# Kernel optimization log

Measured on AMD Instinct MI355X. Metric: run time of the kernel, lower is better.

Reference implementation:

```python
import jax, jax.numpy as jnp
import numpy as np

NEIGHBOR_N = 3


def setup_inputs() -> dict:
    key = jax.random.key(0)
    ks = jax.random.split(key, 4)
    B, D = 8192, 512
    H = D // 2
    sess_emb = jax.random.normal(ks[0], (B, D), dtype=jnp.float32)
    pool_emb = jax.random.normal(ks[1], (1024, D), dtype=jnp.float32)
    # torch Linear default init ~ U(-1/sqrt(fan_in), 1/sqrt(fan_in)); scaled normals ok as baseline
    W1 = jax.random.normal(ks[2], (D, H), dtype=jnp.float32) / np.sqrt(D)
    b1 = jnp.zeros((H,), dtype=jnp.float32)
    W2 = jax.random.normal(ks[3], (H, D), dtype=jnp.float32) / np.sqrt(H)
    b2 = jnp.zeros((D,), dtype=jnp.float32)
    return {"sess_emb": sess_emb, "pool_emb": pool_emb, "W1": W1, "b1": b1, "W2": W2, "b2": b2}


def reference(sess_emb, pool_emb, W1, b1, W2, b2):
    # scoring MLP (dropout = identity in eval mode)
    h = jax.nn.relu(sess_emb @ W1 + b1)          # (B, D/2)
    sess_proj = h @ W2 + b2                       # (B, D)
    # self-similarity and top-k neighbors
    sim_matrix = sess_proj @ sess_proj.T          # (B, B)
    cos_topk, topk_indice = jax.lax.top_k(sim_matrix, NEIGHBOR_N)  # (B, K)
    sess_topk = sess_emb[topk_indice]             # (B, K, D) gather
    cos_topk = jax.nn.softmax(cos_topk, axis=-1)  # (B, K)
    neighbor_sess = jnp.einsum('bk,bkd->bd', cos_topk, sess_topk)  # (B, D)
    return (sess_topk, neighbor_sess, cos_topk)
```

## Files before the change

### kernel.cpp

```cpp
#include <hip/hip_runtime.h>
#include <hip/hip_bf16.h>
#include <math.h>

#define NB 8192
#define DD 512
#define HH 256
#define TB 128
#define BK 32
#define BK2 64
#define KT2 (DD / BK2)
#define NSLOT 64
#define ROWKEYS (NSLOT * 3)
#define NCAND 8
#define NTRI 2080

typedef unsigned short ushortT;
typedef __attribute__((ext_vector_type(8))) short bf16x8;
typedef __attribute__((ext_vector_type(4))) float f32x4;

#define AS1(p) ((const __attribute__((address_space(1))) void*)(p))
#define AS3(p) ((__attribute__((address_space(3))) void*)(p))

__device__ __forceinline__ ushortT bf16rne(float f) {
    unsigned u = __float_as_uint(f);
    unsigned r = u + 0x7FFFu + ((u >> 16) & 1u);
    return (ushortT)(r >> 16);
}
__device__ __forceinline__ float bf16tof(ushortT h) {
    return __uint_as_float(((unsigned)h) << 16);
}

__global__ __launch_bounds__(256)
void prep_kernel(const float* __restrict__ sess, const float* __restrict__ W1,
                 const float* __restrict__ W2,
                 ushortT* __restrict__ sess_hi, ushortT* __restrict__ sess_lo,
                 ushortT* __restrict__ w1t_hi, ushortT* __restrict__ w1t_lo,
                 ushortT* __restrict__ w2t_hi, ushortT* __restrict__ w2t_lo) {
    const int b = blockIdx.x, t = threadIdx.x;
    if (b < 2048) {
        size_t i = (size_t)b * 2048 + t * 8;
        float4 f0 = *(const float4*)&sess[i];
        float4 f1 = *(const float4*)&sess[i + 4];
        float f[8] = {f0.x, f0.y, f0.z, f0.w, f1.x, f1.y, f1.z, f1.w};
        unsigned hp[4], lp[4];
#pragma unroll
        for (int j = 0; j < 4; ++j) {
            ushortT h0 = bf16rne(f[2 * j]), h1 = bf16rne(f[2 * j + 1]);
            ushortT l0 = bf16rne(f[2 * j] - bf16tof(h0));
            ushortT l1 = bf16rne(f[2 * j + 1] - bf16tof(h1));
            hp[j] = (unsigned)h0 | ((unsigned)h1 << 16);
            lp[j] = (unsigned)l0 | ((unsigned)l1 << 16);
        }
        *(uint4*)&sess_hi[i] = *(uint4*)hp;
        *(uint4*)&sess_lo[i] = *(uint4*)lp;
    } else if (b < 2112) {
        int o = (b - 2048) * 2048 + t * 8;
        int k = o >> 8, c = o & 255;
        float4 f0 = *(const float4*)&W1[(size_t)k * 256 + c];
        float4 f1 = *(const float4*)&W1[(size_t)k * 256 + c + 4];
        float f[8] = {f0.x, f0.y, f0.z, f0.w, f1.x, f1.y, f1.z, f1.w};
#pragma unroll
        for (int j = 0; j < 8; ++j) {
            ushortT h = bf16rne(f[j]);
            w1t_hi[(size_t)(c + j) * 512 + k] = h;
            w1t_lo[(size_t)(c + j) * 512 + k] = bf16rne(f[j] - bf16tof(h));
        }
    } else {
        int o = (b - 2112) * 2048 + t * 8;
        int k = o >> 9, c = o & 511;
        float4 f0 = *(const float4*)&W2[(size_t)k * 512 + c];
        float4 f1 = *(const float4*)&W2[(size_t)k * 512 + c + 4];
        float f[8] = {f0.x, f0.y, f0.z, f0.w, f1.x, f1.y, f1.z, f1.w};
#pragma unroll
        for (int j = 0; j < 8; ++j) {
            ushortT h = bf16rne(f[j]);
            w2t_hi[(size_t)(c + j) * 256 + k] = h;
            w2t_lo[(size_t)(c + j) * 256 + k] = bf16rne(f[j] - bf16tof(h));
        }
    }
}

template <int KDIM, int NOUT, int EPI, int TM>
__global__ __launch_bounds__(256)
void mlp_gemm(const ushortT* __restrict__ Ahi, const ushortT* __restrict__ Alo,
              const ushortT* __restrict__ Bhi, const ushortT* __restrict__ Blo,
              const float* __restrict__ bias,
              ushortT* __restrict__ Ohi, ushortT* __restrict__ Olo,
              float* __restrict__ Of, ushortT* __restrict__ Ob) {
    constexpr int AC = TM / 16;
    constexpr int CHUNKS = 2 * AC + 32;
    constexpr int QN = CHUNKS / 4;
    constexpr int BUFS = CHUNKS * 512;
    constexpr int MI = TM / 32;
    __shared__ short gsmem[2 * BUFS];
    const int KTILES = KDIM / BK;
    const int t = threadIdx.x;
    const int w = t >> 6, l = t & 63;
    const int wr = w >> 1, wc = w & 1;
    const int tx = l & 15, tg = l >> 4;
    const int rb = blockIdx.x * TM;
    const int cb = blockIdx.y * 256;

    const int rin = l >> 2;
    const int tgs = (l & 3) ^ ((rin >> 1) & 3);
    const int loff = tx * BK + ((tg ^ ((tx >> 1) & 3)) << 3);

    f32x4 acc[MI][8];
#pragma unroll
    for (int i = 0; i < MI; ++i)
#pragma unroll
        for (int j = 0; j < 8; ++j) acc[i][j] = (f32x4){0.f, 0.f, 0.f, 0.f};

#define GSTAGE(buf, k0v)                                                                     \
    {                                                                                        \
        _Pragma("unroll")                                                                    \
        for (int q = 0; q < QN; ++q) {                                                       \
            int c = w * QN + q;                                                              \
            const ushortT* src; int row; int lofs;                                           \
            if (c < AC)            { src = Ahi; row = rb + c * 16 + rin;             lofs = c * 512; }                  \
            else if (c < 2 * AC)   { src = Alo; row = rb + (c - AC) * 16 + rin;      lofs = c * 512; }                  \
            else if (c < 2*AC+16)  { src = Bhi; row = cb + (c - 2*AC) * 16 + rin;    lofs = c * 512; }                  \
            else                   { src = Blo; row = cb + (c - 2*AC - 16) * 16 + rin; lofs = c * 512; }                \
            const ushortT* g = src + (size_t)row * KDIM + (k0v) + tgs * 8;                   \
            __builtin_amdgcn_global_load_lds(AS1(g), AS3(gsmem + (buf) * BUFS + lofs + l * 8), 16, 0, 0); \
        }                                                                                    \
    }

#define GCOMPUTE(kt)                                                                         \
    {                                                                                        \
        const short* Bu = gsmem + ((kt) & 1) * BUFS;                                         \
        bf16x8 ah[MI], al[MI], bh[8], bl[8];                                                 \
        _Pragma("unroll")                                                                    \
        for (int mi = 0; mi < MI; ++mi) {                                                    \
            ah[mi] = *(const bf16x8*)&Bu[(wr * MI + mi) * 512 + loff];                       \
            al[mi] = *(const bf16x8*)&Bu[AC * 512 + (wr * MI + mi) * 512 + loff];            \
        }                                                                                    \
        _Pragma("unroll")                                                                    \
        for (int nj = 0; nj < 8; ++nj) {                                                     \
            bh[nj] = *(const bf16x8*)&Bu[2 * AC * 512 + (wc * 8 + nj) * 512 + loff];         \
            bl[nj] = *(const bf16x8*)&Bu[(2 * AC + 16) * 512 + (wc * 8 + nj) * 512 + loff];  \
        }                                                                                    \
        asm volatile("s_waitcnt lgkmcnt(0)" ::: "memory");                                   \
        __builtin_amdgcn_sched_barrier(0);                                                   \
        __builtin_amdgcn_s_barrier();                                                        \
        __builtin_amdgcn_sched_barrier(0);                                                   \
        _Pragma("unroll")                                                                    \
        for (int mi = 0; mi < MI; ++mi)                                                      \
            _Pragma("unroll")                                                                \
            for (int nj = 0; nj < 8; ++nj) {                                                 \
                acc[mi][nj] = __builtin_amdgcn_mfma_f32_16x16x32_bf16(ah[mi], bh[nj], acc[mi][nj], 0, 0, 0); \
                acc[mi][nj] = __builtin_amdgcn_mfma_f32_16x16x32_bf16(ah[mi], bl[nj], acc[mi][nj], 0, 0, 0); \
                acc[mi][nj] = __builtin_amdgcn_mfma_f32_16x16x32_bf16(al[mi], bh[nj], acc[mi][nj], 0, 0, 0); \
            }                                                                                \
    }

    GSTAGE(0, 0);
    for (int kt = 0; kt < KTILES - 1; ++kt) {
        GSTAGE((kt + 1) & 1, (kt + 1) * BK);
        if constexpr (TM == 64) { asm volatile("s_waitcnt vmcnt(10)" ::: "memory"); }
        else                    { asm volatile("s_waitcnt vmcnt(9)" ::: "memory"); }
        __builtin_amdgcn_sched_barrier(0);
        __builtin_amdgcn_s_barrier();
        __builtin_amdgcn_sched_barrier(0);
        GCOMPUTE(kt);
    }
    asm volatile("s_waitcnt vmcnt(0)" ::: "memory");
    __builtin_amdgcn_sched_barrier(0);
    __builtin_amdgcn_s_barrier();
    __builtin_amdgcn_sched_barrier(0);
    GCOMPUTE(KTILES - 1);
#undef GSTAGE
#undef GCOMPUTE

#pragma unroll
    for (int mi = 0; mi < MI; ++mi) {
#pragma unroll
        for (int nj = 0; nj < 8; ++nj) {
            int col = cb + wc * 128 + nj * 16 + tx;
            float bv = bias[col];
#pragma unroll
            for (int rr = 0; rr < 4; ++rr) {
                int row = rb + wr * (TM / 2) + mi * 16 + tg * 4 + rr;
                float v = acc[mi][nj][rr] + bv;
                if (EPI == 0) {
                    v = fmaxf(v, 0.f);
                    ushortT h = bf16rne(v);
                    Ohi[(size_t)row * NOUT + col] = h;
                    Olo[(size_t)row * NOUT + col] = bf16rne(v - bf16tof(h));
                } else {
                    Of[(size_t)row * NOUT + col] = v;
                    Ob[(size_t)row * NOUT + col] = bf16rne(v);
                }
            }
        }
    }
}

__device__ __forceinline__ void ins3k(unsigned key, unsigned& k0, unsigned& k1, unsigned& k2) {
    bool g0 = key > k0, g1 = key > k1, g2 = key > k2;
    k2 = g1 ? k1 : (g2 ? key : k2);
    k1 = g0 ? k0 : (g1 ? key : k1);
    k0 = g0 ? key : k0;
}
__device__ __forceinline__ void merge3k(unsigned& a0, unsigned& a1, unsigned& a2,
                                        unsigned b0, unsigned b1, unsigned b2) {
    unsigned m0 = a0 > b0 ? a0 : b0;
    bool c0 = a0 > b0;
    unsigned ca1 = c0 ? a1 : b1;
    unsigned cb0 = c0 ? b0 : a0;
    unsigned ca2 = c0 ? a2 : b2;
    unsigned cb1 = c0 ? b1 : a1;
    bool c1 = ca1 > cb0;
    unsigned m1 = c1 ? ca1 : cb0;
    unsigned x = c1 ? ca2 : ca1;
    unsigned y = c1 ? cb0 : cb1;
    unsigned m2 = x > y ? x : y;
    a0 = m0; a1 = m1; a2 = m2;
}
__device__ __forceinline__ unsigned packkey(float f, unsigned idx) {
    unsigned u = __float_as_uint(f);
    unsigned tt = (unsigned)((int)u >> 31) | 0x80000000u;
    return ((u ^ tt) & 0xFFFFE000u) | (8191u - idx);
}

__global__ __launch_bounds__(256)
void sim_mfma_kernel(const short* __restrict__ projb, unsigned* __restrict__ pkeys) {
    const int b = blockIdx.x;
    const int L = (b & 7) * 260 + (b >> 3);
    int jbk = (int)((sqrtf(8.0f * L + 1.0f) - 1.0f) * 0.5f);
    while ((jbk + 1) * (jbk + 2) / 2 <= L) ++jbk;
    while (jbk * (jbk + 1) / 2 > L) --jbk;
    const int ib = L - jbk * (jbk + 1) / 2;
    const bool do_tr = (ib < jbk);

    __shared__ short smem[2 * TB * BK2 * 2];
    short* As = smem;
    short* Bs = smem + 2 * TB * BK2;
    unsigned* evu = (unsigned*)smem;
    unsigned* evt = (unsigned*)smem + 3200;

    const int t = threadIdx.x;
    const int w = t >> 6, l = t & 63;
    const int wr = w >> 1, wc = w & 1;
    const int tx = l & 15, tg = l >> 4;
    const int rb = ib * TB;
    const int jb = jbk * TB;

    const int sl8 = (((l & 7) ^ (l >> 3)) << 3);
    const int sw0 = (((0 + tg) ^ (tx & 7)) << 3);
    const int sw1 = (((4 + tg) ^ (tx & 7)) << 3);

    f32x4 acc[4][4];
#pragma unroll
    for (int i = 0; i < 4; ++i)
#pragma unroll
        for (int j = 0; j < 4; ++j) acc[i][j] = (f32x4){0.f, 0.f, 0.f, 0.f};

#define STAGE(buf, k0)                                                                      \
    {                                                                                       \
        _Pragma("unroll")                                                                   \
        for (int q = 0; q < 4; ++q) {                                                       \
            int c = w * 4 + q;                                                              \
            const short* ga = projb + (size_t)(rb + c * 8 + (l >> 3)) * DD + (k0) + sl8;    \
            __builtin_amdgcn_global_load_lds(AS1(ga), AS3(As + (buf) * 8192 + c * 512 + l * 8), 16, 0, 0); \
            const short* gb = projb + (size_t)(jb + c * 8 + (l >> 3)) * DD + (k0) + sl8;    \
            __builtin_amdgcn_global_load_lds(AS1(gb), AS3(Bs + (buf) * 8192 + c * 512 + l * 8), 16, 0, 0); \
        }                                                                                   \
    }

#define COMPUTE(kt)                                                                          \
    {                                                                                        \
        const short* Ab = As + ((kt) & 1) * 8192;                                            \
        const short* Bb = Bs + ((kt) & 1) * 8192;                                            \
        bf16x8 af0[4], af1[4], bf0[4], bf1[4];                                               \
        _Pragma("unroll")                                                                    \
        for (int mi = 0; mi < 4; ++mi) {                                                     \
            int row = wr * 64 + mi * 16 + tx;                                                \
            af0[mi] = *(const bf16x8*)&Ab[row * 64 + sw0];                                   \
            af1[mi] = *(const bf16x8*)&Ab[row * 64 + sw1];                                   \
        }                                                                                    \
        _Pragma("unroll")                                                                    \
        for (int nj = 0; nj < 4; ++nj) {                                                     \
            int row = wc * 64 + nj * 16 + tx;                                                \
            bf0[nj] = *(const bf16x8*)&Bb[row * 64 + sw0];                                   \
            bf1[nj] = *(const bf16x8*)&Bb[row * 64 + sw1];                                   \
        }                                                                                    \
        asm volatile("s_waitcnt lgkmcnt(0)" ::: "memory");                                   \
        __builtin_amdgcn_sched_barrier(0);                                                   \
        __builtin_amdgcn_s_barrier();                                                        \
        __builtin_amdgcn_sched_barrier(0);                                                   \
        _Pragma("unroll")                                                                    \
        for (int mi = 0; mi < 4; ++mi)                                                       \
            _Pragma("unroll")                                                                \
            for (int nj = 0; nj < 4; ++nj)                                                   \
                acc[mi][nj] = __builtin_amdgcn_mfma_f32_16x16x32_bf16(af0[mi], bf0[nj], acc[mi][nj], 0, 0, 0); \
        _Pragma("unroll")                                                                    \
        for (int mi = 0; mi < 4; ++mi)                                                       \
            _Pragma("unroll")                                                                \
            for (int nj = 0; nj < 4; ++nj)                                                   \
                acc[mi][nj] = __builtin_amdgcn_mfma_f32_16x16x32_bf16(af1[mi], bf1[nj], acc[mi][nj], 0, 0, 0); \
    }

    STAGE(0, 0);
    for (int kt = 0; kt < KT2 - 1; ++kt) {
        STAGE((kt + 1) & 1, (kt + 1) * BK2);
        asm volatile("s_waitcnt vmcnt(8)" ::: "memory");
        __builtin_amdgcn_sched_barrier(0);
        __builtin_amdgcn_s_barrier();
        __builtin_amdgcn_sched_barrier(0);
        COMPUTE(kt);
    }
    asm volatile("s_waitcnt vmcnt(0)" ::: "memory");
    __builtin_amdgcn_sched_barrier(0);
    __builtin_amdgcn_s_barrier();
    __builtin_amdgcn_sched_barrier(0);
    COMPUTE(KT2 - 1);
#undef STAGE
#undef COMPUTE

    __syncthreads();

    unsigned cinv[4];
#pragma unroll
    for (int nj = 0; nj < 4; ++nj)
        cinv[nj] = 8191u - (unsigned)(jb + wc * 64 + nj * 16 + tx);
#pragma unroll
    for (int mi = 0; mi < 4; ++mi) {
#pragma unroll
        for (int rr = 0; rr < 4; ++rr) {
            unsigned k0 = 0, k1 = 0, k2 = 0;
#pragma unroll
            for (int nj = 0; nj < 4; ++nj) {
                unsigned u = __float_as_uint(acc[mi][nj][rr]);
                unsigned tt = (unsigned)((int)u >> 31) | 0x80000000u;
                ins3k(((u ^ tt) & 0xFFFFE000u) | cinv[nj], k0, k1, k2);
            }
#pragma unroll
            for (int s = 1; s <= 2; s <<= 1) {
                unsigned b0 = (unsigned)__shfl_xor((int)k0, s, 64);
                unsigned b1 = (unsigned)__shfl_xor((int)k1, s, 64);
                unsigned b2 = (unsigned)__shfl_xor((int)k2, s, 64);
                merge3k(k0, k1, k2, b0, b1, b2);
            }
            if ((tx & 3) == 0) {
                int lrow = wr * 64 + mi * 16 + tg * 4 + rr;
                unsigned* e = &evu[lrow * 25 + (wc * 4 + (tx >> 2)) * 3];
                e[0] = k0; e[1] = k1; e[2] = k2;
            }
        }
    }

    if (do_tr) {
#pragma unroll
        for (int nj = 0; nj < 4; ++nj) {
            unsigned k0 = 0, k1 = 0, k2 = 0;
#pragma unroll
            for (int mi = 0; mi < 4; ++mi) {
#pragma unroll
                for (int rr = 0; rr < 4; ++rr) {
                    unsigned idx = (unsigned)(rb + wr * 64 + mi * 16 + tg * 4 + rr);
                    ins3k(packkey(acc[mi][nj][rr], idx), k0, k1, k2);
                }
            }
#pragma unroll
            for (int s = 16; s <= 32; s <<= 1) {
                unsigned b0 = (unsigned)__shfl_xor((int)k0, s, 64);
                unsigned b1 = (unsigned)__shfl_xor((int)k1, s, 64);
                unsigned b2 = (unsigned)__shfl_xor((int)k2, s, 64);
                merge3k(k0, k1, k2, b0, b1, b2);
            }
            if (tg == 0) {
                int col = wc * 64 + nj * 16 + tx;
                unsigned* e = &evt[col * 6 + wr * 3];
                e[0] = k0; e[1] = k1; e[2] = k2;
            }
        }
    }
    __syncthreads();

    if (t < TB) {
        unsigned k0 = 0, k1 = 0, k2 = 0;
        const unsigned* e = &evu[t * 25];
#pragma unroll
        for (int s = 0; s < 24; ++s) ins3k(e[s], k0, k1, k2);
        unsigned* pk = pkeys + (size_t)(rb + t) * ROWKEYS + jbk * 3;
        pk[0] = k0; pk[1] = k1; pk[2] = k2;
    }
    if (do_tr && t < TB) {
        unsigned k0 = 0, k1 = 0, k2 = 0;
        const unsigned* e = &evt[t * 6];
#pragma unroll
        for (int s = 0; s < 6; ++s) ins3k(e[s], k0, k1, k2);
        unsigned* pk = pkeys + (size_t)(jb + t) * ROWKEYS + ib * 3;
        pk[0] = k0; pk[1] = k1; pk[2] = k2;
    }
}

__global__ __launch_bounds__(256)
void rerank_out_kernel(const float* __restrict__ proj, const unsigned* __restrict__ pkeys,
                       const float* __restrict__ sess, float* __restrict__ out,
                       float* __restrict__ cos_out) {
    int r = blockIdx.x * 4 + (threadIdx.x >> 6);
    int t = threadIdx.x & 63;
    const unsigned* pk = pkeys + (size_t)r * ROWKEYS;
    unsigned a0 = pk[3 * t], a1 = pk[3 * t + 1], a2 = pk[3 * t + 2];
    {
        unsigned m01 = a0 > a1 ? a0 : a1, n01 = a0 > a1 ? a1 : a0;
        unsigned m2 = n01 > a2 ? n01 : a2, n2 = n01 > a2 ? a2 : n01;
        a0 = m01 > m2 ? m01 : m2;
        a1 = m01 > m2 ? m2 : m01;
        a2 = n2;
    }
    unsigned ck[NCAND];
#pragma unroll
    for (int i = 0; i < NCAND; ++i) {
        unsigned m = a0;
#pragma unroll
        for (int s = 1; s < 64; s <<= 1) {
            unsigned o = (unsigned)__shfl_xor((int)m, s, 64);
            m = m > o ? m : o;
        }
        ck[i] = m;
        if (a0 == m) { a0 = a1; a1 = a2; a2 = 0; }
    }
    int cj[NCAND];
#pragma unroll
    for (int i = 0; i < NCAND; ++i) cj[i] = 8191 - (int)(ck[i] & 0x1FFFu);

    const float* pr = proj + (size_t)r * DD;
    float myp[8];
#pragma unroll
    for (int k = 0; k < 8; ++k) myp[k] = pr[t * 8 + k];
    double part[NCAND];
#pragma unroll
    for (int i = 0; i < NCAND; ++i) {
        const float* pc = proj + (size_t)cj[i] * DD;
        double s = 0.0;
#pragma unroll
        for (int k = 0; k < 8; ++k) s += (double)myp[k] * (double)pc[t * 8 + k];
        part[i] = s;
    }
#pragma unroll
    for (int i = 0; i < NCAND; ++i) {
#pragma unroll
        for (int s = 1; s < 64; s <<= 1) part[i] += __shfl_xor(part[i], s, 64);
    }
    double bv0 = -1e300, bv1 = -1e300, bv2 = -1e300;
    int bj0 = 0x7fffffff, bj1 = 0x7fffffff, bj2 = 0x7fffffff;
#pragma unroll
    for (int i = 0; i < NCAND; ++i) {
        double v = part[i]; int j = cj[i];
        bool g2 = (v > bv2) || (v == bv2 && j < bj2);
        bool g1 = (v > bv1) || (v == bv1 && j < bj1);
        bool g0 = (v > bv0) || (v == bv0 && j < bj0);
        if (g2) {
            if (g1) {
                if (g0) { bv2 = bv1; bj2 = bj1; bv1 = bv0; bj1 = bj0; bv0 = v; bj0 = j; }
                else    { bv2 = bv1; bj2 = bj1; bv1 = v; bj1 = j; }
            } else      { bv2 = v; bj2 = j; }
        }
    }
    double e1 = exp(bv1 - bv0), e2 = exp(bv2 - bv0);
    double inv = 1.0 / (1.0 + e1 + e2);
    float w0 = (float)inv, w1 = (float)(e1 * inv), w2 = (float)(e2 * inv);
    if (t == 0) {
        cos_out[r * 3 + 0] = w0; cos_out[r * 3 + 1] = w1; cos_out[r * 3 + 2] = w2;
    }
    const float4* s0 = (const float4*)(sess + (size_t)bj0 * DD);
    const float4* s1 = (const float4*)(sess + (size_t)bj1 * DD);
    const float4* s2 = (const float4*)(sess + (size_t)bj2 * DD);
    float4* o = (float4*)(out + (size_t)r * 3 * DD);
    float4* nb = (float4*)(out + (size_t)NB * 3 * DD + (size_t)r * DD);
#pragma unroll
    for (int e = 0; e < 2; ++e) {
        int q = t + e * 64;
        float4 x0 = s0[q], x1 = s1[q], x2 = s2[q];
        o[q] = x0; o[128 + q] = x1; o[256 + q] = x2;
        float4 v;
        v.x = fmaf(w0, x0.x, fmaf(w1, x1.x, w2 * x2.x));
        v.y = fmaf(w0, x0.y, fmaf(w1, x1.y, w2 * x2.y));
        v.z = fmaf(w0, x0.z, fmaf(w1, x1.z, w2 * x2.z));
        v.w = fmaf(w0, x0.w, fmaf(w1, x1.w, w2 * x2.w));
        nb[q] = v;
    }
}

extern "C" void kernel_launch(void* const* d_in, const int* in_sizes, int n_in,
                              void* d_out, int out_size, void* d_ws, size_t ws_size,
                              hipStream_t stream) {
    const float* sess = (const float*)d_in[0];
    const float* W1 = (const float*)d_in[2];
    const float* b1 = (const float*)d_in[3];
    const float* W2 = (const float*)d_in[4];
    const float* b2 = (const float*)d_in[5];
    float* out = (float*)d_out;

    const size_t MBc = 1u << 20;
    char* W = (char*)d_ws;
    float*   proj    = (float*)W;
    ushortT* sess_hi = (ushortT*)W;
    ushortT* sess_lo = sess_hi + (size_t)NB * DD;
    ushortT* projb   = (ushortT*)(W + 16 * MBc);
    ushortT* h_hi    = (ushortT*)(W + 24 * MBc);
    ushortT* h_lo    = (ushortT*)(W + 28 * MBc);
    ushortT* w1t_hi  = (ushortT*)(W + 32 * MBc);
    ushortT* w1t_lo  = w1t_hi + 256 * 512;
    ushortT* w2t_hi  = w1t_lo + 256 * 512;
    ushortT* w2t_lo  = w2t_hi + 512 * 256;
    unsigned* pkeys  = (unsigned*)(W + 24 * MBc);

    float* cos_out = out + (size_t)NB * 3 * DD + (size_t)NB * DD;

    hipLaunchKernelGGL(prep_kernel, dim3(2176), dim3(256), 0, stream,
                       sess, W1, W2, sess_hi, sess_lo, w1t_hi, w1t_lo, w2t_hi, w2t_lo);
    hipLaunchKernelGGL((mlp_gemm<512, 256, 0, 32>), dim3(NB / 32, 1), dim3(256), 0, stream,
                       sess_hi, sess_lo, w1t_hi, w1t_lo, b1, h_hi, h_lo, (float*)nullptr, (ushortT*)nullptr);
    hipLaunchKernelGGL((mlp_gemm<256, 512, 1, 64>), dim3(NB / 64, 2), dim3(256), 0, stream,
                       h_hi, h_lo, w2t_hi, w2t_lo, b2, (ushortT*)nullptr, (ushortT*)nullptr, proj, projb);
    hipLaunchKernelGGL(sim_mfma_kernel, dim3(NTRI), dim3(256), 0, stream,
                       (const short*)projb, pkeys);
    hipLaunchKernelGGL(rerank_out_kernel, dim3(NB / 4), dim3(256), 0, stream,
                       proj, pkeys, sess, out, cos_out);
}
```

Before: 141.9 us.

## Halve sim GEMM K-tile to 32 and use supertile block ordering

The similarity GEMM now stages K slices of 32 instead of 64, which halves LDS use per buffer and changes the swizzle to match the narrower rows. It also replaces the linear triangular tile index with a blocked order over 8x8 super-tiles, so nearby blocks reuse the same row panels in L2. The aim is more resident blocks per CU and better cache locality. In exchange there are twice as many barrier and stage iterations, with fewer MFMAs between each sync.

```diff
diff --git a/kernel.cpp b/kernel.cpp
--- a/kernel.cpp
+++ b/kernel.cpp
@@ -7,8 +7,7 @@
 #define HH 256
 #define TB 128
 #define BK 32
-#define BK2 64
-#define KT2 (DD / BK2)
+#define KTS (DD / BK)
 #define NSLOT 64
 #define ROWKEYS (NSLOT * 3)
 #define NCAND 8
@@ -227,15 +226,26 @@
 void sim_mfma_kernel(const short* __restrict__ projb, unsigned* __restrict__ pkeys) {
     const int b = blockIdx.x;
     const int L = (b & 7) * 260 + (b >> 3);
-    int jbk = (int)((sqrtf(8.0f * L + 1.0f) - 1.0f) * 0.5f);
-    while ((jbk + 1) * (jbk + 2) / 2 <= L) ++jbk;
-    while (jbk * (jbk + 1) / 2 > L) --jbk;
-    const int ib = L - jbk * (jbk + 1) / 2;
+    int rem = L, si = 0, sj = 0;
+    for (;;) {
+        int n = (si == sj) ? 36 : 64;
+        if (rem < n) break;
+        rem -= n;
+        if (si == sj) { si = 0; ++sj; } else { ++si; }
+    }
+    int ci, cj;
+    if (si == sj) {
+        cj = 0;
+        while (rem >= cj + 1) { rem -= cj + 1; ++cj; }
+        ci = rem;
+    } else { ci = rem & 7; cj = rem >> 3; }
+    const int ib = si * 8 + ci;
+    const int jbk = sj * 8 + cj;
     const bool do_tr = (ib < jbk);
 
-    __shared__ short smem[2 * TB * BK2 * 2];
+    __shared__ short smem[2 * TB * BK * 2];
     short* As = smem;
-    short* Bs = smem + 2 * TB * BK2;
+    short* Bs = smem + 2 * TB * BK;
     unsigned* evu = (unsigned*)smem;
     unsigned* evt = (unsigned*)smem + 3200;
 
@@ -246,9 +256,9 @@
     const int rb = ib * TB;
     const int jb = jbk * TB;
 
-    const int sl8 = (((l & 7) ^ (l >> 3)) << 3);
-    const int sw0 = (((0 + tg) ^ (tx & 7)) << 3);
-    const int sw1 = (((4 + tg) ^ (tx & 7)) << 3);
+    const int rin = l >> 2;
+    const int tgs = (l & 3) ^ ((rin >> 1) & 3);
+    const int loff = tx * BK + ((tg ^ ((tx >> 1) & 3)) << 3);
 
     f32x4 acc[4][4];
 #pragma unroll
@@ -259,32 +269,26 @@
 #define STAGE(buf, k0)                                                                      \
     {                                                                                       \
         _Pragma("unroll")                                                                   \
-        for (int q = 0; q < 4; ++q) {                                                       \
-            int c = w * 4 + q;                                                              \
-            const short* ga = projb + (size_t)(rb + c * 8 + (l >> 3)) * DD + (k0) + sl8;    \
-            __builtin_amdgcn_global_load_lds(AS1(ga), AS3(As + (buf) * 8192 + c * 512 + l * 8), 16, 0, 0); \
-            const short* gb = projb + (size_t)(jb + c * 8 + (l >> 3)) * DD + (k0) + sl8;    \
-            __builtin_amdgcn_global_load_lds(AS1(gb), AS3(Bs + (buf) * 8192 + c * 512 + l * 8), 16, 0, 0); \
+        for (int q = 0; q < 2; ++q) {                                                       \
+            int c = w * 2 + q;                                                              \
+            const short* ga = projb + (size_t)(rb + c * 16 + rin) * DD + (k0) + tgs * 8;    \
+            __builtin_amdgcn_global_load_lds(AS1(ga), AS3(As + (buf) * (TB * BK) + c * 512 + l * 8), 16, 0, 0); \
+            const short* gb = projb + (size_t)(jb + c * 16 + rin) * DD + (k0) + tgs * 8;    \
+            __builtin_amdgcn_global_load_lds(AS1(gb), AS3(Bs + (buf) * (TB * BK) + c * 512 + l * 8), 16, 0, 0); \
         }                                                                                   \
     }
 
 #define COMPUTE(kt)                                                                          \
     {                                                                                        \
-        const short* Ab = As + ((kt) & 1) * 8192;                                            \
-        const short* Bb = Bs + ((kt) & 1) * 8192;                                            \
-        bf16x8 af0[4], af1[4], bf0[4], bf1[4];                                               \
-        _Pragma("unroll")                                                                    \
-        for (int mi = 0; mi < 4; ++mi) {                                                     \
-            int row = wr * 64 + mi * 16 + tx;                                                \
-            af0[mi] = *(const bf16x8*)&Ab[row * 64 + sw0];                                   \
-            af1[mi] = *(const bf16x8*)&Ab[row * 64 + sw1];                                   \
-        }                                                                                    \
-        _Pragma("unroll")                                                                    \
-        for (int nj = 0; nj < 4; ++nj) {                                                     \
-            int row = wc * 64 + nj * 16 + tx;                                                \
-            bf0[nj] = *(const bf16x8*)&Bb[row * 64 + sw0];                                   \
-            bf1[nj] = *(const bf16x8*)&Bb[row * 64 + sw1];                                   \
-        }                                                                                    \
+        const short* Ab = As + ((kt) & 1) * (TB * BK);                                       \
+        const short* Bb = Bs + ((kt) & 1) * (TB * BK);                                       \
+        bf16x8 af[4], bfr[4];                                                                \
+        _Pragma("unroll")                                                                    \
+        for (int mi = 0; mi < 4; ++mi)                                                       \
+            af[mi] = *(const bf16x8*)&Ab[(wr * 64 + mi * 16) * BK + loff];                   \
+        _Pragma("unroll")                                                                    \
+        for (int nj = 0; nj < 4; ++nj)                                                       \
+            bfr[nj] = *(const bf16x8*)&Bb[(wc * 64 + nj * 16) * BK + loff];                  \
         asm volatile("s_waitcnt lgkmcnt(0)" ::: "memory");                                   \
         __builtin_amdgcn_sched_barrier(0);                                                   \
         __builtin_amdgcn_s_barrier();                                                        \
@@ -293,18 +297,13 @@
         for (int mi = 0; mi < 4; ++mi)                                                       \
             _Pragma("unroll")                                                                \
             for (int nj = 0; nj < 4; ++nj)                                                   \
-                acc[mi][nj] = __builtin_amdgcn_mfma_f32_16x16x32_bf16(af0[mi], bf0[nj], acc[mi][nj], 0, 0, 0); \
-        _Pragma("unroll")                                                                    \
-        for (int mi = 0; mi < 4; ++mi)                                                       \
-            _Pragma("unroll")                                                                \
-            for (int nj = 0; nj < 4; ++nj)                                                   \
-                acc[mi][nj] = __builtin_amdgcn_mfma_f32_16x16x32_bf16(af1[mi], bf1[nj], acc[mi][nj], 0, 0, 0); \
+                acc[mi][nj] = __builtin_amdgcn_mfma_f32_16x16x32_bf16(af[mi], bfr[nj], acc[mi][nj], 0, 0, 0); \
     }
 
     STAGE(0, 0);
-    for (int kt = 0; kt < KT2 - 1; ++kt) {
-        STAGE((kt + 1) & 1, (kt + 1) * BK2);
-        asm volatile("s_waitcnt vmcnt(8)" ::: "memory");
+    for (int kt = 0; kt < KTS - 1; ++kt) {
+        STAGE((kt + 1) & 1, (kt + 1) * BK);
+        asm volatile("s_waitcnt vmcnt(4)" ::: "memory");
         __builtin_amdgcn_sched_barrier(0);
         __builtin_amdgcn_s_barrier();
         __builtin_amdgcn_sched_barrier(0);
@@ -314,7 +313,7 @@
     __builtin_amdgcn_sched_barrier(0);
     __builtin_amdgcn_s_barrier();
     __builtin_amdgcn_sched_barrier(0);
-    COMPUTE(KT2 - 1);
+    COMPUTE(KTS - 1);
 #undef STAGE
 #undef COMPUTE
 
```

Result: slower. 146.5 us (+3.2%).
